# Kernel tuning notes

Hardware: AMD Instinct MI355X
Metric: run time of the kernel (lower is better)

The kernel has to match this reference:

```python
import jax, jax.numpy as jnp
import numpy as np


def setup_inputs() -> dict:
    key = jax.random.key(0)
    k1, k2 = jax.random.split(key)
    query_features = jax.random.normal(k1, (8, 2048, 256), dtype=jnp.float32)   # (B, S, D)
    support_weights = jax.random.normal(k2, (20, 256), dtype=jnp.float32)       # (N, D)
    return {"query_features": query_features, "support_weights": support_weights}


def reference(query_features, support_weights):
    # Original: transpose query to (B, D, S), repeat channels n_cls times,
    # grouped conv1d with groups = n_cls*D, group_size=1, kernel_size=1, padding=0.
    # That is exactly a per-(class, channel) scale of the query features.
    B, S, D = query_features.shape
    N = support_weights.shape[0]
    q = jnp.transpose(query_features, (0, 2, 1))            # (B, D, S)
    # out[b, n, c, s] = q[b, c, s] * w[n, c]
    out = q[:, None, :, :] * support_weights[None, :, :, None]  # (B, N, D, S)
    return out.reshape(B * N, D, S)                          # (B*N, D, S)
```

## Files before the change

### kernel.cpp

```cpp
#include <hip/hip_runtime.h>


namespace {
constexpr int kB = 8;
constexpr int kS = 2048;
constexpr int kD = 256;
constexpr int kN = 20;
constexpr int TS = 64;
constexpr int TC = 64;
constexpr int PAD_TS = TS + 4;
}

__global__ __launch_bounds__(256)
void frw_kernel(const float* __restrict__ q, const float* __restrict__ w,
                float* __restrict__ out) {
  const int s0 = blockIdx.x * TS;
  const int c0 = blockIdx.y * TC;
  const int b  = blockIdx.z;
  const int t  = threadIdx.x;

  __shared__ float tile[TC][PAD_TS];
  __shared__ float ws[kN][TC];

  for (int i = t; i < kN * TC; i += 256) {
    const int n  = i / TC;
    const int cc = i % TC;
    ws[n][cc] = w[n * kD + c0 + cc];
  }

  const int lane16 = t & 15;
  const int grp16  = t >> 4;

  {
    const int cvec = lane16 * 4;
    for (int k = 0; k < 4; ++k) {
      const int srow = grp16 + k * 16;
      const float4 v = *reinterpret_cast<const float4*>(
          &q[((size_t)b * kS + (size_t)(s0 + srow)) * kD + (c0 + cvec)]);
      tile[cvec + 0][srow] = v.x;
      tile[cvec + 1][srow] = v.y;
      tile[cvec + 2][srow] = v.z;
      tile[cvec + 3][srow] = v.w;
    }
  }
  __syncthreads();

  const int svec = lane16 * 4;
  for (int k = 0; k < 4; ++k) {
    const int cc = grp16 + k * 16;
    const int c  = c0 + cc;
    const float4 v = *reinterpret_cast<const float4*>(&tile[cc][svec]);
    size_t idx = ((size_t)b * kN * kD + (size_t)c) * kS + (size_t)(s0 + svec);
    for (int n = 0; n < kN; ++n) {
      const float sc = ws[n][cc];
      float4 o;
      o.x = v.x * sc;
      o.y = v.y * sc;
      o.z = v.z * sc;
      o.w = v.w * sc;
      *reinterpret_cast<float4*>(&out[idx]) = o;
      idx += (size_t)kD * kS;
    }
  }
}

extern "C" void kernel_launch(void* const* d_in, const int* in_sizes, int n_in,
                              void* d_out, int out_size, void* d_ws, size_t ws_size,
                              hipStream_t stream) {
  const float* q = (const float*)d_in[0];
  const float* w = (const float*)d_in[1];
  float* out = (float*)d_out;

  dim3 grid(kS / TS, kD / TC, kB);
  frw_kernel<<<grid, 256, 0, stream>>>(q, w, out);
}
```

Before: 346.1 us.

## Reshape tiles to long sequence rows and reorder output write loop

```diff
diff --git a/kernel.cpp b/kernel.cpp
--- a/kernel.cpp
+++ b/kernel.cpp
@@ -6,9 +6,9 @@
 constexpr int kS = 2048;
 constexpr int kD = 256;
 constexpr int kN = 20;
-constexpr int TS = 64;
-constexpr int TC = 64;
-constexpr int PAD_TS = TS + 4;
+constexpr int TS = 512;
+constexpr int TC = 16;
+constexpr int PTS = TS + 4;
 }
 
 __global__ __launch_bounds__(256)
@@ -19,7 +19,7 @@
   const int b  = blockIdx.z;
   const int t  = threadIdx.x;
 
-  __shared__ float tile[TC][PAD_TS];
+  __shared__ float tile[TC][PTS];
   __shared__ float ws[kN][TC];
 
   for (int i = t; i < kN * TC; i += 256) {
@@ -28,38 +28,39 @@
     ws[n][cc] = w[n * kD + c0 + cc];
   }
 
-  const int lane16 = t & 15;
-  const int grp16  = t >> 4;
-
   {
-    const int cvec = lane16 * 4;
-    for (int k = 0; k < 4; ++k) {
-      const int srow = grp16 + k * 16;
+    const int lane4 = t & 3;
+    const int srow  = t >> 2;
+    const int cvec  = lane4 * 4;
+#pragma unroll
+    for (int k = 0; k < 8; ++k) {
+      const int ss = srow + k * 64;
       const float4 v = *reinterpret_cast<const float4*>(
-          &q[((size_t)b * kS + (size_t)(s0 + srow)) * kD + (c0 + cvec)]);
-      tile[cvec + 0][srow] = v.x;
-      tile[cvec + 1][srow] = v.y;
-      tile[cvec + 2][srow] = v.z;
-      tile[cvec + 3][srow] = v.w;
+          &q[((size_t)b * kS + (size_t)(s0 + ss)) * kD + (c0 + cvec)]);
+      tile[cvec + 0][ss] = v.x;
+      tile[cvec + 1][ss] = v.y;
+      tile[cvec + 2][ss] = v.z;
+      tile[cvec + 3][ss] = v.w;
     }
   }
   __syncthreads();
 
-  const int svec = lane16 * 4;
-  for (int k = 0; k < 4; ++k) {
-    const int cc = grp16 + k * 16;
-    const int c  = c0 + cc;
-    const float4 v = *reinterpret_cast<const float4*>(&tile[cc][svec]);
-    size_t idx = ((size_t)b * kN * kD + (size_t)c) * kS + (size_t)(s0 + svec);
-    for (int n = 0; n < kN; ++n) {
-      const float sc = ws[n][cc];
+  const int half = t >> 7;
+  const int soff = (t & 127) * 4;
+  for (int n = 0; n < kN; ++n) {
+    const size_t base_bn = ((size_t)(b * kN + n)) * kD;
+#pragma unroll
+    for (int rg = 0; rg < TC / 2; ++rg) {
+      const int r = rg * 2 + half;
+      const float sc = ws[n][r];
+      const float4 v = *reinterpret_cast<const float4*>(&tile[r][soff]);
       float4 o;
       o.x = v.x * sc;
       o.y = v.y * sc;
       o.z = v.z * sc;
       o.w = v.w * sc;
-      *reinterpret_cast<float4*>(&out[idx]) = o;
-      idx += (size_t)kD * kS;
+      *reinterpret_cast<float4*>(
+          &out[(base_bn + (size_t)(c0 + r)) * kS + (size_t)(s0 + soff)]) = o;
     }
   }
 }
```

Result: no change. 340.7 us (-1.6%).
